# Kernel tuning notes

Hardware: AMD Instinct MI355X
Metric: run time of the kernel (lower is better)

## Reference

```python
import math
import jax, jax.numpy as jnp
import numpy as np

DEGREE = 5
LN_EPS = 1e-5


def hermite_psi(C, r):
    # x_d = tanh(linspace(-1,1,C)) * (sqrt(2r+1)+1), shape [C]
    x_d = jnp.tanh(jnp.linspace(-1.0, 1.0, C)) * (math.sqrt(2 * r + 1) + 1.0)
    g = jnp.exp(-x_d ** 2 / 2.0)
    rows = [math.pi ** (-0.25) * g]
    if r > 0:
        rows.append(math.sqrt(2.0) * math.pi ** (-0.25) * x_d * g)
    for k in range(2, r + 1):
        rows.append(math.sqrt(2.0 / k) * x_d * rows[-1] - math.sqrt((k - 1) / k) * rows[-2])
    return jnp.stack(rows)  # [r+1, C]


def setup_inputs() -> dict:
    key = jax.random.key(0)
    k1, k2 = jax.random.split(key)
    B, C, H, W = 16, 512, 64, 64
    O = 512
    x = jax.random.normal(k1, (B, C, H, W), dtype=jnp.float32)
    ln_w = jnp.ones((C,), dtype=jnp.float32)
    ln_b = jnp.zeros((C,), dtype=jnp.float32)
    fc_w = jax.random.normal(k2, (O, C), dtype=jnp.float32) * (1.0 / math.sqrt(C))
    fc_b = jnp.zeros((O,), dtype=jnp.float32)
    return {"x": x, "ln_w": ln_w, "ln_b": ln_b, "fc_w": fc_w, "fc_b": fc_b}


def reference(x, ln_w, ln_b, fc_w, fc_b):
    B, C, H, W = x.shape
    O = fc_w.shape[0]
    # [B, HW, C]
    q = x.reshape(B, C, H * W).transpose(0, 2, 1)
    # LayerNorm over channels (biased variance, eps=1e-5)
    mu = q.mean(axis=-1, keepdims=True)
    var = ((q - mu) ** 2).mean(axis=-1, keepdims=True)
    q = (q - mu) / jnp.sqrt(var + LN_EPS) * ln_w + ln_b
    # Constant Hermite basis [r+1, C]
    psi = hermite_psi(C, DEGREE).astype(x.dtype)
    # Tiny cross-attention: scores [B, HW, r+1]
    scores = jnp.einsum('bnc,rc->bnr', q, psi) / math.sqrt(C)
    attn = jax.nn.softmax(scores, axis=-1)
    y = jnp.einsum('bnr,rc->bnc', attn, psi)  # [B, HW, C]
    # 1x1 conv == pointwise GEMM over channels
    out = jnp.einsum('bnc,oc->bon', y, fc_w) + fc_b[None, :, None]
    return out.reshape(B, O, H, W)
```

## Files before the change

kernel.cpp:

```cpp
#include <hip/hip_runtime.h>
#include <math.h>

#define C 512
#define NPIX 4096
#define BATCH 16
#define O 512
#define R 6
#define LN_EPS 1e-5f

typedef float vf2 __attribute__((ext_vector_type(2)));


__device__ __forceinline__ void hermite_rows(int c, float rows[R]) {
    float t = -1.0f + 2.0f * (float)c / 511.0f;
    float xd = tanhf(t) * 4.31662479035539984911f;
    float g = expf(-0.5f * xd * xd);
    const float pi_m14 = 0.75112554446494248286f;
    rows[0] = pi_m14 * g;
    rows[1] = 1.41421356237309504880f * pi_m14 * xd * g;
    #pragma unroll
    for (int k = 2; k <= 5; ++k)
        rows[k] = sqrtf(2.0f / k) * xd * rows[k - 1] - sqrtf((k - 1.0f) / k) * rows[k - 2];
}

__global__ __launch_bounds__(64) void setup_all(const float* __restrict__ lnw,
                                                const float* __restrict__ lnb,
                                                const float* __restrict__ fcw,
                                                const float* __restrict__ fcb,
                                                float* __restrict__ ws) {
    const int o = blockIdx.x;
    const int l = threadIdx.x;
    if (o < O) {
        float acc[R] = {0.f, 0.f, 0.f, 0.f, 0.f, 0.f};
        #pragma unroll
        for (int k = 0; k < 8; ++k) {
            int c = l + (k << 6);
            float rows[R];
            hermite_rows(c, rows);
            float w = fcw[o * C + c];
            #pragma unroll
            for (int r = 0; r < R; ++r) acc[r] += rows[r] * w;
        }
        #pragma unroll
        for (int r = 0; r < R; ++r)
            #pragma unroll
            for (int m = 32; m >= 1; m >>= 1) acc[r] += __shfl_xor(acc[r], m, 64);
        if (l == 0) {
            float bias = fcb[o];
            float* M = ws + 4112 + o * 8;
            #pragma unroll
            for (int r = 0; r < R; ++r) M[r] = acc[r] + bias;
        }
    } else {
        float sw[R] = {0.f, 0.f, 0.f, 0.f, 0.f, 0.f};
        float sb[R] = {0.f, 0.f, 0.f, 0.f, 0.f, 0.f};
        #pragma unroll
        for (int k = 0; k < 8; ++k) {
            int c = l + (k << 6);
            float rows[R];
            hermite_rows(c, rows);
            float w = lnw[c], bb = lnb[c];
            float* dst = ws + c * 8;
            #pragma unroll
            for (int r = 0; r < R; ++r) {
                float rw = rows[r] * w;
                dst[r] = rw;
                sw[r] += rw;
                sb[r] += rows[r] * bb;
            }
        }
        #pragma unroll
        for (int r = 0; r < R; ++r) {
            #pragma unroll
            for (int m = 32; m >= 1; m >>= 1) {
                sw[r] += __shfl_xor(sw[r], m, 64);
                sb[r] += __shfl_xor(sb[r], m, 64);
            }
        }
        if (l == 0) {
            #pragma unroll
            for (int r = 0; r < R; ++r) { ws[4096 + r] = sw[r]; ws[4104 + r] = sb[r]; }
        }
    }
}

__global__ __launch_bounds__(1024, 4) void fused_kernel(const float* __restrict__ x,
                                                        const float* __restrict__ ws,
                                                        float* __restrict__ out) {
    __shared__ float part[16][8][128];
    __shared__ float attn_s[R][128];
    const int tid = threadIdx.x;
    const int wv = tid >> 6;
    const int l = tid & 63;
    const int b = blockIdx.x >> 4;
    const int sg = blockIdx.x & 15;
    const int n0 = sg << 8;
    const int p2 = l << 1;
    const int wuni = __builtin_amdgcn_readfirstlane(wv);

    const float* xw = x + (((size_t)(b * C + (wuni << 5))) << 12);
    float* ow = out + (((size_t)(b * O + (wuni << 5))) << 12);
    const float* wbase = ws + ((size_t)(wuni << 5) << 3);
    const float* Ms = ws + 4112 + ((size_t)(wuni << 5) << 3);

    float sx, sy, ssx, ssy;
    float a0x, a0y, a1x, a1y, a2x, a2y, a3x, a3y, a4x, a4y, a5x, a5y;

    {
        const float* xb = xw + n0 + p2;
        sx = sy = ssx = ssy = 0.f;
        a0x = a0y = a1x = a1y = a2x = a2y = 0.f;
        a3x = a3y = a4x = a4y = a5x = a5y = 0.f;
        #pragma unroll
        for (int i = 0; i < 32; ++i) {
            vf2 xv = *(const vf2*)(xb + ((size_t)i << 12));
            const float* wr = wbase + (i << 3);
            float w0 = wr[0], w1 = wr[1], w2 = wr[2];
            float w3 = wr[3], w4 = wr[4], w5 = wr[5];
            sx += xv.x;          sy += xv.y;
            ssx += xv.x * xv.x;  ssy += xv.y * xv.y;
            a0x += xv.x * w0;    a0y += xv.y * w0;
            a1x += xv.x * w1;    a1y += xv.y * w1;
            a2x += xv.x * w2;    a2y += xv.y * w2;
            a3x += xv.x * w3;    a3y += xv.y * w3;
            a4x += xv.x * w4;    a4y += xv.y * w4;
            a5x += xv.x * w5;    a5y += xv.y * w5;
        }
        vf2 t;
        t.x = sx;  t.y = sy;  *(vf2*)&part[wv][0][p2] = t;
        t.x = ssx; t.y = ssy; *(vf2*)&part[wv][1][p2] = t;
        t.x = a0x; t.y = a0y; *(vf2*)&part[wv][2][p2] = t;
        t.x = a1x; t.y = a1y; *(vf2*)&part[wv][3][p2] = t;
        t.x = a2x; t.y = a2y; *(vf2*)&part[wv][4][p2] = t;
        t.x = a3x; t.y = a3y; *(vf2*)&part[wv][5][p2] = t;
        t.x = a4x; t.y = a4y; *(vf2*)&part[wv][6][p2] = t;
        t.x = a5x; t.y = a5y; *(vf2*)&part[wv][7][p2] = t;
    }
    __syncthreads();

    if (tid < 128) {
        float v[8];
        #pragma unroll
        for (int st = 0; st < 8; ++st) {
            float acc = 0.f;
            #pragma unroll
            for (int w = 0; w < 16; ++w) acc += part[w][st][tid];
            v[st] = acc;
        }
        float mu = v[0] * (1.0f / 512.0f);
        float var = v[1] * (1.0f / 512.0f) - mu * mu;
        float rsig = rsqrtf(var + LN_EPS);
        const float invsq = 0.04419417382415922f;
        float sc[R], mx = -1e30f;
        #pragma unroll
        for (int r = 0; r < R; ++r) {
            float swp = ws[4096 + r], sbp = ws[4104 + r];
            sc[r] = ((v[2 + r] - mu * swp) * rsig + sbp) * invsq;
            mx = fmaxf(mx, sc[r]);
        }
        float es = 0.f, at[R];
        #pragma unroll
        for (int r = 0; r < R; ++r) { at[r] = expf(sc[r] - mx); es += at[r]; }
        float inv = 1.0f / es;
        #pragma unroll
        for (int r = 0; r < R; ++r) attn_s[r][tid] = at[r] * inv;
    }
    __syncthreads();

    float arx[R], ary[R];
    #pragma unroll
    for (int r = 0; r < R; ++r) {
        vf2 a = *(const vf2*)&attn_s[r][p2];
        arx[r] = a.x; ary[r] = a.y;
    }

    {
        const float* xb = xw + n0 + 128 + p2;
        float* ob = ow + n0 + p2;
        sx = sy = ssx = ssy = 0.f;
        a0x = a0y = a1x = a1y = a2x = a2y = 0.f;
        a3x = a3y = a4x = a4y = a5x = a5y = 0.f;
        #pragma unroll
        for (int i = 0; i < 32; ++i) {
            vf2 xv = *(const vf2*)(xb + ((size_t)i << 12));
            const float* mo = Ms + (i << 3);
            float m0 = mo[0], m1 = mo[1], m2 = mo[2];
            float m3 = mo[3], m4 = mo[4], m5 = mo[5];
            vf2 res;
            res.x = arx[0] * m0 + arx[1] * m1 + arx[2] * m2
                  + arx[3] * m3 + arx[4] * m4 + arx[5] * m5;
            res.y = ary[0] * m0 + ary[1] * m1 + ary[2] * m2
                  + ary[3] * m3 + ary[4] * m4 + ary[5] * m5;
            __builtin_nontemporal_store(res, (vf2*)(ob + ((size_t)i << 12)));
            const float* wr = wbase + (i << 3);
            float w0 = wr[0], w1 = wr[1], w2 = wr[2];
            float w3 = wr[3], w4 = wr[4], w5 = wr[5];
            sx += xv.x;          sy += xv.y;
            ssx += xv.x * xv.x;  ssy += xv.y * xv.y;
            a0x += xv.x * w0;    a0y += xv.y * w0;
            a1x += xv.x * w1;    a1y += xv.y * w1;
            a2x += xv.x * w2;    a2y += xv.y * w2;
            a3x += xv.x * w3;    a3y += xv.y * w3;
            a4x += xv.x * w4;    a4y += xv.y * w4;
            a5x += xv.x * w5;    a5y += xv.y * w5;
        }
        vf2 t;
        t.x = sx;  t.y = sy;  *(vf2*)&part[wv][0][p2] = t;
        t.x = ssx; t.y = ssy; *(vf2*)&part[wv][1][p2] = t;
        t.x = a0x; t.y = a0y; *(vf2*)&part[wv][2][p2] = t;
        t.x = a1x; t.y = a1y; *(vf2*)&part[wv][3][p2] = t;
        t.x = a2x; t.y = a2y; *(vf2*)&part[wv][4][p2] = t;
        t.x = a3x; t.y = a3y; *(vf2*)&part[wv][5][p2] = t;
        t.x = a4x; t.y = a4y; *(vf2*)&part[wv][6][p2] = t;
        t.x = a5x; t.y = a5y; *(vf2*)&part[wv][7][p2] = t;
    }
    __syncthreads();

    if (tid < 128) {
        float v[8];
        #pragma unroll
        for (int st = 0; st < 8; ++st) {
            float acc = 0.f;
            #pragma unroll
            for (int w = 0; w < 16; ++w) acc += part[w][st][tid];
            v[st] = acc;
        }
        float mu = v[0] * (1.0f / 512.0f);
        float var = v[1] * (1.0f / 512.0f) - mu * mu;
        float rsig = rsqrtf(var + LN_EPS);
        const float invsq = 0.04419417382415922f;
        float sc[R], mx = -1e30f;
        #pragma unroll
        for (int r = 0; r < R; ++r) {
            float swp = ws[4096 + r], sbp = ws[4104 + r];
            sc[r] = ((v[2 + r] - mu * swp) * rsig + sbp) * invsq;
            mx = fmaxf(mx, sc[r]);
        }
        float es = 0.f, at[R];
        #pragma unroll
        for (int r = 0; r < R; ++r) { at[r] = expf(sc[r] - mx); es += at[r]; }
        float inv = 1.0f / es;
        #pragma unroll
        for (int r = 0; r < R; ++r) attn_s[r][tid] = at[r] * inv;
    }
    __syncthreads();

    #pragma unroll
    for (int r = 0; r < R; ++r) {
        vf2 a = *(const vf2*)&attn_s[r][p2];
        arx[r] = a.x; ary[r] = a.y;
    }

    {
        float* ob = ow + n0 + 128 + p2;
        #pragma unroll
        for (int j = 0; j < 32; ++j) {
            const float* mo = Ms + (j << 3);
            float m0 = mo[0], m1 = mo[1], m2 = mo[2];
            float m3 = mo[3], m4 = mo[4], m5 = mo[5];
            vf2 res;
            res.x = arx[0] * m0 + arx[1] * m1 + arx[2] * m2
                  + arx[3] * m3 + arx[4] * m4 + arx[5] * m5;
            res.y = ary[0] * m0 + ary[1] * m1 + ary[2] * m2
                  + ary[3] * m3 + ary[4] * m4 + ary[5] * m5;
            __builtin_nontemporal_store(res, (vf2*)(ob + ((size_t)j << 12)));
        }
    }
}

extern "C" void kernel_launch(void* const* d_in, const int* in_sizes, int n_in,
                              void* d_out, int out_size, void* d_ws, size_t ws_size,
                              hipStream_t stream) {
    const float* x    = (const float*)d_in[0];
    const float* ln_w = (const float*)d_in[1];
    const float* ln_b = (const float*)d_in[2];
    const float* fc_w = (const float*)d_in[3];
    const float* fc_b = (const float*)d_in[4];
    float* out = (float*)d_out;
    float* ws = (float*)d_ws;

    setup_all<<<O + 1, 64, 0, stream>>>(ln_w, ln_b, fc_w, fc_b, ws);
    fused_kernel<<<BATCH * 16, 1024, 0, stream>>>(x, ws, out);
}
```

Measured before the change: 247.1 us.

## Warp-specialize middle phase: half waves load next tile, half write outputs

In the middle phase the block now splits its waves. Waves 0-7 read all 512 channels for the second pixel tile, 64 channels each. Waves 8-15 write the output for the first tile, 64 output channels each. This replaces the old scheme where every wave interleaved loads and stores over 32 channels. The activation loads also become nontemporal. The change tries to separate read and write streams so they overlap without contention, at the cost of a longer per-wave loop and possible imbalance between the two wave groups.

```diff
diff --git a/kernel.cpp b/kernel.cpp
--- a/kernel.cpp
+++ b/kernel.cpp
@@ -88,32 +88,32 @@
                                                         const float* __restrict__ ws,
                                                         float* __restrict__ out) {
     __shared__ float part[16][8][128];
-    __shared__ float attn_s[R][128];
+    __shared__ float attn_s[2][R][128];
     const int tid = threadIdx.x;
     const int wv = tid >> 6;
     const int l = tid & 63;
     const int b = blockIdx.x >> 4;
-    const int sg = blockIdx.x & 15;
-    const int n0 = sg << 8;
+    const int st = blockIdx.x & 15;
+    const int nA = st << 8;
+    const int nB = nA + 128;
     const int p2 = l << 1;
     const int wuni = __builtin_amdgcn_readfirstlane(wv);
 
-    const float* xw = x + (((size_t)(b * C + (wuni << 5))) << 12);
-    float* ow = out + (((size_t)(b * O + (wuni << 5))) << 12);
-    const float* wbase = ws + ((size_t)(wuni << 5) << 3);
-    const float* Ms = ws + 4112 + ((size_t)(wuni << 5) << 3);
+    const float* xrow = x + (((size_t)(b * C)) << 12);
+    float* orow = out + (((size_t)(b * O)) << 12);
 
     float sx, sy, ssx, ssy;
     float a0x, a0y, a1x, a1y, a2x, a2y, a3x, a3y, a4x, a4y, a5x, a5y;
 
     {
-        const float* xb = xw + n0 + p2;
+        const float* xb = xrow + (((size_t)(wuni << 5)) << 12) + nA + p2;
+        const float* wbase = ws + ((size_t)(wuni << 5) << 3);
         sx = sy = ssx = ssy = 0.f;
         a0x = a0y = a1x = a1y = a2x = a2y = 0.f;
         a3x = a3y = a4x = a4y = a5x = a5y = 0.f;
         #pragma unroll
         for (int i = 0; i < 32; ++i) {
-            vf2 xv = *(const vf2*)(xb + ((size_t)i << 12));
+            vf2 xv = __builtin_nontemporal_load((const vf2*)(xb + ((size_t)i << 12)));
             const float* wr = wbase + (i << 3);
             float w0 = wr[0], w1 = wr[1], w2 = wr[2];
             float w3 = wr[3], w4 = wr[4], w5 = wr[5];
@@ -141,11 +141,11 @@
     if (tid < 128) {
         float v[8];
         #pragma unroll
-        for (int st = 0; st < 8; ++st) {
+        for (int s = 0; s < 8; ++s) {
             float acc = 0.f;
             #pragma unroll
-            for (int w = 0; w < 16; ++w) acc += part[w][st][tid];
-            v[st] = acc;
+            for (int w = 0; w < 16; ++w) acc += part[w][s][tid];
+            v[s] = acc;
         }
         float mu = v[0] * (1.0f / 512.0f);
         float var = v[1] * (1.0f / 512.0f) - mu * mu;
@@ -163,35 +163,19 @@
         for (int r = 0; r < R; ++r) { at[r] = expf(sc[r] - mx); es += at[r]; }
         float inv = 1.0f / es;
         #pragma unroll
-        for (int r = 0; r < R; ++r) attn_s[r][tid] = at[r] * inv;
-    }
-    __syncthreads();
-
-    float arx[R], ary[R];
-    #pragma unroll
-    for (int r = 0; r < R; ++r) {
-        vf2 a = *(const vf2*)&attn_s[r][p2];
-        arx[r] = a.x; ary[r] = a.y;
-    }
-
-    {
-        const float* xb = xw + n0 + 128 + p2;
-        float* ob = ow + n0 + p2;
+        for (int r = 0; r < R; ++r) attn_s[0][r][tid] = at[r] * inv;
+    }
+    __syncthreads();
+
+    if (wv < 8) {
+        const float* xb = xrow + (((size_t)(wuni << 6)) << 12) + nB + p2;
+        const float* wbase = ws + ((size_t)(wuni << 6) << 3);
         sx = sy = ssx = ssy = 0.f;
         a0x = a0y = a1x = a1y = a2x = a2y = 0.f;
         a3x = a3y = a4x = a4y = a5x = a5y = 0.f;
-        #pragma unroll
-        for (int i = 0; i < 32; ++i) {
-            vf2 xv = *(const vf2*)(xb + ((size_t)i << 12));
-            const float* mo = Ms + (i << 3);
-            float m0 = mo[0], m1 = mo[1], m2 = mo[2];
-            float m3 = mo[3], m4 = mo[4], m5 = mo[5];
-            vf2 res;
-            res.x = arx[0] * m0 + arx[1] * m1 + arx[2] * m2
-                  + arx[3] * m3 + arx[4] * m4 + arx[5] * m5;
-            res.y = ary[0] * m0 + ary[1] * m1 + ary[2] * m2
-                  + ary[3] * m3 + ary[4] * m4 + ary[5] * m5;
-            __builtin_nontemporal_store(res, (vf2*)(ob + ((size_t)i << 12)));
+        #pragma unroll 8
+        for (int i = 0; i < 64; ++i) {
+            vf2 xv = __builtin_nontemporal_load((const vf2*)(xb + ((size_t)i << 12)));
             const float* wr = wbase + (i << 3);
             float w0 = wr[0], w1 = wr[1], w2 = wr[2];
             float w3 = wr[3], w4 = wr[4], w5 = wr[5];
@@ -213,17 +197,39 @@
         t.x = a3x; t.y = a3y; *(vf2*)&part[wv][5][p2] = t;
         t.x = a4x; t.y = a4y; *(vf2*)&part[wv][6][p2] = t;
         t.x = a5x; t.y = a5y; *(vf2*)&part[wv][7][p2] = t;
+    } else {
+        float arx[R], ary[R];
+        #pragma unroll
+        for (int r = 0; r < R; ++r) {
+            vf2 a = *(const vf2*)&attn_s[0][r][p2];
+            arx[r] = a.x; ary[r] = a.y;
+        }
+        const int w8 = wuni - 8;
+        const float* Ms = ws + 4112 + ((size_t)(w8 << 6) << 3);
+        float* ob = orow + (((size_t)(w8 << 6)) << 12) + nA + p2;
+        #pragma unroll 8
+        for (int j = 0; j < 64; ++j) {
+            const float* mo = Ms + (j << 3);
+            float m0 = mo[0], m1 = mo[1], m2 = mo[2];
+            float m3 = mo[3], m4 = mo[4], m5 = mo[5];
+            vf2 res;
+            res.x = arx[0] * m0 + arx[1] * m1 + arx[2] * m2
+                  + arx[3] * m3 + arx[4] * m4 + arx[5] * m5;
+            res.y = ary[0] * m0 + ary[1] * m1 + ary[2] * m2
+                  + ary[3] * m3 + ary[4] * m4 + ary[5] * m5;
+            __builtin_nontemporal_store(res, (vf2*)(ob + ((size_t)j << 12)));
+        }
     }
     __syncthreads();
 
     if (tid < 128) {
         float v[8];
         #pragma unroll
-        for (int st = 0; st < 8; ++st) {
+        for (int s = 0; s < 8; ++s) {
             float acc = 0.f;
             #pragma unroll
-            for (int w = 0; w < 16; ++w) acc += part[w][st][tid];
-            v[st] = acc;
+            for (int w = 0; w < 8; ++w) acc += part[w][s][tid];
+            v[s] = acc;
         }
         float mu = v[0] * (1.0f / 512.0f);
         float var = v[1] * (1.0f / 512.0f) - mu * mu;
@@ -241,18 +247,19 @@
         for (int r = 0; r < R; ++r) { at[r] = expf(sc[r] - mx); es += at[r]; }
         float inv = 1.0f / es;
         #pragma unroll
-        for (int r = 0; r < R; ++r) attn_s[r][tid] = at[r] * inv;
-    }
-    __syncthreads();
-
-    #pragma unroll
-    for (int r = 0; r < R; ++r) {
-        vf2 a = *(const vf2*)&attn_s[r][p2];
-        arx[r] = a.x; ary[r] = a.y;
-    }
+        for (int r = 0; r < R; ++r) attn_s[1][r][tid] = at[r] * inv;
+    }
+    __syncthreads();
 
     {
-        float* ob = ow + n0 + 128 + p2;
+        float arx[R], ary[R];
+        #pragma unroll
+        for (int r = 0; r < R; ++r) {
+            vf2 a = *(const vf2*)&attn_s[1][r][p2];
+            arx[r] = a.x; ary[r] = a.y;
+        }
+        const float* Ms = ws + 4112 + ((size_t)(wuni << 5) << 3);
+        float* ob = orow + (((size_t)(wuni << 5)) << 12) + nB + p2;
         #pragma unroll
         for (int j = 0; j < 32; ++j) {
             const float* mo = Ms + (j << 3);
```

Result: faster. 231.3 us (-6.4%).
